# Performance work log

Hardware: AMD Instinct MI355X
Metric: run time of the kernel (lower is better)

## Reference

```python
import jax, jax.numpy as jnp
import numpy as np

N_NODES = 50000
N_EDGES = 800000
D_IN = 128
D_HID = 256
D_OUT = 256


def setup_inputs() -> dict:
    key = jax.random.key(0)
    ks = jax.random.split(key, 16)
    x = jax.random.normal(ks[0], (N_NODES, D_IN), dtype=jnp.float32)
    src = jax.random.randint(ks[1], (N_EDGES,), 0, N_NODES)
    dst = jax.random.randint(ks[2], (N_EDGES,), 0, N_NODES)

    def w(k, fan_in, fan_out):
        return jax.random.normal(k, (fan_in, fan_out), dtype=jnp.float32) / np.sqrt(fan_in)

    return {
        "x": x, "src": src, "dst": dst,
        "Ws0": w(ks[3], D_IN, D_HID), "Wn0": w(ks[4], D_IN, D_HID), "b0": jnp.zeros((D_HID,), jnp.float32),
        "Ws1": w(ks[5], D_HID, D_HID), "Wn1": w(ks[6], D_HID, D_HID), "b1": jnp.zeros((D_HID,), jnp.float32),
        "Ws2": w(ks[7], D_HID, D_OUT), "Wn2": w(ks[8], D_HID, D_OUT), "b2": jnp.zeros((D_OUT,), jnp.float32),
    }


def _sage_layer(h, src, dst, Ws, Wn, b, n_nodes):
    # mean aggregation: gather src features per edge, segment-sum into dst, divide by in-degree
    msg_sum = jax.ops.segment_sum(h[src], dst, num_segments=n_nodes)          # [N, d]
    deg = jax.ops.segment_sum(jnp.ones((src.shape[0],), h.dtype), dst, num_segments=n_nodes)
    h_neigh = msg_sum / jnp.maximum(deg, 1.0)[:, None]                        # zero in-degree -> 0
    return jax.nn.relu(h @ Ws + h_neigh @ Wn + b)


def reference(x, src, dst, Ws0, Wn0, b0, Ws1, Wn1, b1, Ws2, Wn2, b2):
    n = x.shape[0]
    h = _sage_layer(x, src, dst, Ws0, Wn0, b0, n)
    h = _sage_layer(h, src, dst, Ws1, Wn1, b1, n)
    h = _sage_layer(h, src, dst, Ws2, Wn2, b2, n)
    return h
```

## Files before the change

### kernel.cpp

```cpp
#include <hip/hip_runtime.h>
#include <hip/hip_bf16.h>

#define NN 50000
#define NE 800000
#define NB 782
#define BCAP 1536
#define OVFCAP 4096
#define RADIX_BLOCKS 128

typedef __attribute__((ext_vector_type(8))) _Float16 half8v;
typedef __attribute__((ext_vector_type(4))) _Float16 half4v;
typedef __attribute__((ext_vector_type(2))) _Float16 half2v;
typedef __attribute__((ext_vector_type(4))) float f32x4;

__device__ __forceinline__ void gload_lds16(const void* g, void* l) {
  __builtin_amdgcn_global_load_lds((const __attribute__((address_space(1))) void*)g,
                                   (__attribute__((address_space(3))) void*)l, 16, 0, 0);
}
__device__ __forceinline__ void vm_wait5() {
  asm volatile("s_waitcnt vmcnt(5)" ::: "memory");
  __builtin_amdgcn_sched_barrier(0);
}
__device__ __forceinline__ void vm_wait0() {
  asm volatile("s_waitcnt vmcnt(0)" ::: "memory");
  __builtin_amdgcn_sched_barrier(0);
}
__device__ __forceinline__ void barx() {
  __builtin_amdgcn_sched_barrier(0);
  __builtin_amdgcn_s_barrier();
  __builtin_amdgcn_sched_barrier(0);
}

__global__ void k_zero(int* __restrict__ p, int n) {
  int i = blockIdx.x * blockDim.x + threadIdx.x;
  if (i < n) p[i] = 0;
}

__global__ __launch_bounds__(256) void k_radix(const int* __restrict__ src,
                                               const int* __restrict__ dst,
                                               int* __restrict__ bcur,
                                               uint* __restrict__ pairs,
                                               int* __restrict__ cnt,
                                               int* __restrict__ ovfn,
                                               uint* __restrict__ ovf) {
  __shared__ int hist[NB];
  __shared__ int lbase[NB];
  const int tid = threadIdx.x;
  const int chunk = (NE + RADIX_BLOCKS - 1) / RADIX_BLOCKS;
  const int e0 = blockIdx.x * chunk;
  const int e1 = min(e0 + chunk, NE);
  for (int i = tid; i < NB; i += 256) hist[i] = 0;
  __syncthreads();
  for (int e = e0 + tid; e < e1; e += 256) atomicAdd(&hist[dst[e] >> 6], 1);
  __syncthreads();
  for (int i = tid; i < NB; i += 256) {
    int h = hist[i];
    lbase[i] = h ? atomicAdd(&bcur[i], h) : 0;
    hist[i] = 0;
  }
  __syncthreads();
  for (int e = e0 + tid; e < e1; e += 256) {
    int d = dst[e], s = src[e];
    int b = d >> 6;
    int p = lbase[b] + atomicAdd(&hist[b], 1);
    if (p < BCAP) {
      pairs[(size_t)b * BCAP + p] = ((uint)s << 6) | (uint)(d & 63);
    } else {
      int oi = atomicAdd(ovfn, 1);
      if (oi < OVFCAP) ovf[oi] = ((uint)d << 16) | (uint)s;
      atomicAdd(&cnt[d], 1);
    }
  }
}

__global__ __launch_bounds__(256) void k_countb(const int* __restrict__ bcur,
                                                const uint* __restrict__ pairs,
                                                int* __restrict__ cnt) {
  __shared__ int lc[64];
  const int b = blockIdx.x;
  if (threadIdx.x < 64) lc[threadIdx.x] = 0;
  __syncthreads();
  const int m = min(bcur[b], BCAP);
  for (int e = threadIdx.x; e < m; e += 256)
    atomicAdd(&lc[pairs[(size_t)b * BCAP + e] & 63], 1);
  __syncthreads();
  if (threadIdx.x < 64) {
    int node = b * 64 + threadIdx.x;
    int v = lc[threadIdx.x];
    if (node < NN && v) atomicAdd(&cnt[node], v);
  }
}

__global__ __launch_bounds__(1024) void k_scan(int* __restrict__ cnt, int* __restrict__ rowptr) {
  __shared__ int wsum[16];
  __shared__ int woff[16];
  __shared__ int tot;
  const int tid = threadIdx.x;
  const int lane = tid & 63;
  const int w = tid >> 6;
  int running = 0;
  for (int base = 0; base < NN; base += 4096) {
    const int i4 = (base >> 2) + tid;
    int4 v = make_int4(0, 0, 0, 0);
    if (i4 * 4 < NN) v = reinterpret_cast<const int4*>(cnt)[i4];
    const int tsum = v.x + v.y + v.z + v.w;
    int x = tsum;
#pragma unroll
    for (int off = 1; off < 64; off <<= 1) {
      int t = __shfl_up(x, off);
      if (lane >= off) x += t;
    }
    if (lane == 63) wsum[w] = x;
    __syncthreads();
    if (w == 0) {
      int s = (lane < 16) ? wsum[lane] : 0;
#pragma unroll
      for (int off = 1; off < 16; off <<= 1) {
        int t = __shfl_up(s, off);
        if (lane >= off) s += t;
      }
      if (lane < 16) woff[lane] = s - wsum[lane];
      if (lane == 15) tot = s;
    }
    __syncthreads();
    if (i4 * 4 < NN) {
      int excl = running + woff[w] + (x - tsum);
      int4 r;
      r.x = excl;
      r.y = excl + v.x;
      r.z = r.y + v.y;
      r.w = r.z + v.z;
      reinterpret_cast<int4*>(rowptr)[i4] = r;
      reinterpret_cast<int4*>(cnt)[i4] = r;
    }
    running += tot;
    __syncthreads();
  }
  if (tid == 0) rowptr[NN] = running;
}

__global__ __launch_bounds__(256) void k_fillb(const int* __restrict__ bcur,
                                               const uint* __restrict__ pairs,
                                               int* __restrict__ cursor,
                                               int* __restrict__ col) {
  const int b = blockIdx.x;
  const int m = min(bcur[b], BCAP);
  for (int e = threadIdx.x; e < m; e += 256) {
    uint u = pairs[(size_t)b * BCAP + e];
    int node = b * 64 + (int)(u & 63);
    int p = atomicAdd(&cursor[node], 1);
    col[p] = (int)(u >> 6);
  }
}

__global__ void k_fillovf(const int* __restrict__ ovfn, const uint* __restrict__ ovf,
                          int* __restrict__ cursor, int* __restrict__ col) {
  int n = min(*ovfn, OVFCAP);
  for (int i = threadIdx.x; i < n; i += 256) {
    uint u = ovf[i];
    int p = atomicAdd(&cursor[u >> 16], 1);
    col[p] = (int)(u & 0xFFFFu);
  }
}

__global__ void k_wpack(const float* __restrict__ W, _Float16* __restrict__ Wp, int K) {
  int t = blockIdx.x * blockDim.x + threadIdx.x;
  if (t >= K * 32) return;
  int l = t & 63;
  int c = (t >> 6) & 15;
  int kb = t >> 10;
  int row = c * 16 + (l & 15);
  int k = kb * 32 + (l >> 4) * 8;
  half8v o;
#pragma unroll
  for (int i = 0; i < 8; ++i) o[i] = (_Float16)W[(size_t)(k + i) * 256 + row];
  *reinterpret_cast<half8v*>(Wp + (size_t)t * 8) = o;
}

__global__ void k_split16(const float* __restrict__ x, _Float16* __restrict__ X16) {
  int t = blockIdx.x * blockDim.x + threadIdx.x;
  if (t >= NN * 16) return;
  const float* p = x + (size_t)t * 8;
  float4 v0 = *reinterpret_cast<const float4*>(p);
  float4 v1 = *reinterpret_cast<const float4*>(p + 4);
  half8v o;
  o[0] = (_Float16)v0.x; o[1] = (_Float16)v0.y; o[2] = (_Float16)v0.z; o[3] = (_Float16)v0.w;
  o[4] = (_Float16)v1.x; o[5] = (_Float16)v1.y; o[6] = (_Float16)v1.z; o[7] = (_Float16)v1.w;
  *reinterpret_cast<half8v*>(X16 + (size_t)t * 8) = o;
}

__global__ __launch_bounds__(256) void k_agg_x16(const float* __restrict__ x,
                                                 const int* __restrict__ rowptr,
                                                 const int* __restrict__ col,
                                                 _Float16* __restrict__ N) {
  const int lane = threadIdx.x & 63;
  const int n = blockIdx.x * 4 + (threadIdx.x >> 6);
  if (n >= NN) return;
  const int start = rowptr[n];
  const int end = rowptr[n + 1];
  float a0 = 0.f, a1 = 0.f;
  for (int base = start; base < end; base += 64) {
    int e = base + lane;
    int c = (e < end) ? col[e] : 0;
    int m = min(64, end - base);
    int t = 0;
    for (; t + 3 < m; t += 4) {
      int c0 = __shfl(c, t), c1 = __shfl(c, t + 1), c2 = __shfl(c, t + 2), c3 = __shfl(c, t + 3);
      float2 v0 = *reinterpret_cast<const float2*>(x + (size_t)c0 * 128 + lane * 2);
      float2 v1 = *reinterpret_cast<const float2*>(x + (size_t)c1 * 128 + lane * 2);
      float2 v2 = *reinterpret_cast<const float2*>(x + (size_t)c2 * 128 + lane * 2);
      float2 v3 = *reinterpret_cast<const float2*>(x + (size_t)c3 * 128 + lane * 2);
      a0 += v0.x + v1.x + v2.x + v3.x;
      a1 += v0.y + v1.y + v2.y + v3.y;
    }
    for (; t < m; ++t) {
      int cs = __shfl(c, t);
      float2 v = *reinterpret_cast<const float2*>(x + (size_t)cs * 128 + lane * 2);
      a0 += v.x;
      a1 += v.y;
    }
  }
  int deg = end - start;
  float sc = 1.0f / (float)(deg > 0 ? deg : 1);
  half2v o;
  o[0] = (_Float16)(a0 * sc);
  o[1] = (_Float16)(a1 * sc);
  *reinterpret_cast<half2v*>(N + (size_t)n * 128 + lane * 2) = o;
}

__global__ __launch_bounds__(256) void k_agg16(const _Float16* __restrict__ H,
                                               const int* __restrict__ rowptr,
                                               const int* __restrict__ col,
                                               _Float16* __restrict__ N) {
  const int lane = threadIdx.x & 63;
  const int n = blockIdx.x * 4 + (threadIdx.x >> 6);
  if (n >= NN) return;
  const int start = rowptr[n];
  const int end = rowptr[n + 1];
  float a0 = 0.f, a1 = 0.f, a2 = 0.f, a3 = 0.f;
  for (int base = start; base < end; base += 64) {
    int e = base + lane;
    int c = (e < end) ? col[e] : 0;
    int m = min(64, end - base);
    int t = 0;
    for (; t + 3 < m; t += 4) {
      int c0 = __shfl(c, t), c1 = __shfl(c, t + 1), c2 = __shfl(c, t + 2), c3 = __shfl(c, t + 3);
      half4v v0 = *reinterpret_cast<const half4v*>(H + (size_t)c0 * 256 + lane * 4);
      half4v v1 = *reinterpret_cast<const half4v*>(H + (size_t)c1 * 256 + lane * 4);
      half4v v2 = *reinterpret_cast<const half4v*>(H + (size_t)c2 * 256 + lane * 4);
      half4v v3 = *reinterpret_cast<const half4v*>(H + (size_t)c3 * 256 + lane * 4);
      a0 += (float)v0[0] + (float)v1[0] + (float)v2[0] + (float)v3[0];
      a1 += (float)v0[1] + (float)v1[1] + (float)v2[1] + (float)v3[1];
      a2 += (float)v0[2] + (float)v1[2] + (float)v2[2] + (float)v3[2];
      a3 += (float)v0[3] + (float)v1[3] + (float)v2[3] + (float)v3[3];
    }
    for (; t < m; ++t) {
      int cs = __shfl(c, t);
      half4v v = *reinterpret_cast<const half4v*>(H + (size_t)cs * 256 + lane * 4);
      a0 += (float)v[0];
      a1 += (float)v[1];
      a2 += (float)v[2];
      a3 += (float)v[3];
    }
  }
  int deg = end - start;
  float sc = 1.0f / (float)(deg > 0 ? deg : 1);
  half4v o;
  o[0] = (_Float16)(a0 * sc);
  o[1] = (_Float16)(a1 * sc);
  o[2] = (_Float16)(a2 * sc);
  o[3] = (_Float16)(a3 * sc);
  *reinterpret_cast<half4v*>(N + (size_t)n * 256 + lane * 4) = o;
}

__global__ __launch_bounds__(256) void k_mfma16(
    const _Float16* __restrict__ A1, const _Float16* __restrict__ A2,
    const _Float16* __restrict__ W1p, const _Float16* __restrict__ W2p,
    const float* __restrict__ bias, int K,
    _Float16* __restrict__ outH, float* __restrict__ outF) {
  __shared__ _Float16 LDS[20480];
  const int tid = threadIdx.x;
  const int w = tid >> 6;
  const int lane = tid & 63;
  const int lrow = lane & 15;
  const int kg8 = (lane >> 4) * 8;
  const int m0 = blockIdx.x * 64;
  const int nk = K >> 5;
  const int nsteps = nk * 2;

  f32x4 acc[4][4];
#pragma unroll
  for (int i = 0; i < 4; ++i)
#pragma unroll
    for (int j = 0; j < 4; ++j) acc[i][j] = (f32x4){0.f, 0.f, 0.f, 0.f};

  int arowi = m0 + w * 16 + lrow;
  const size_t arow = (size_t)(arowi < NN ? arowi : NN - 1);

#define STAGE(S, B)                                                            \
  {                                                                            \
    const _Float16* Ap = ((S) >= nk) ? A2 : A1;                                \
    const _Float16* Wp = ((S) >= nk) ? W2p : W1p;                              \
    const int sl = ((S) >= nk) ? (S) - nk : (S);                               \
    gload_lds16(Ap + arow * K + (sl << 5) + kg8,                               \
                (void*)&LDS[(B) * 10240 + w * 512]);                           \
    const _Float16* wsrc = Wp + (size_t)(sl * 16 + w * 4) * 512 + lane * 8;    \
    _Pragma("unroll") for (int j = 0; j < 4; ++j)                              \
        gload_lds16(wsrc + j * 512,                                            \
                    (void*)&LDS[(B) * 10240 + 2048 + (w * 4 + j) * 512]);      \
  }

#define COMPUTE(B)                                                             \
  {                                                                            \
    half8v af[4];                                                              \
    _Pragma("unroll") for (int rf = 0; rf < 4; ++rf)                           \
        af[rf] = *reinterpret_cast<const half8v*>(                             \
            &LDS[(B) * 10240 + rf * 512 + lane * 8]);                          \
    _Pragma("unroll") for (int cf = 0; cf < 4; ++cf) {                         \
      half8v bf = *reinterpret_cast<const half8v*>(                            \
          &LDS[(B) * 10240 + 2048 + (w * 4 + cf) * 512 + lane * 8]);           \
      _Pragma("unroll") for (int rf = 0; rf < 4; ++rf)                         \
          acc[rf][cf] = __builtin_amdgcn_mfma_f32_16x16x32_f16(                \
              af[rf], bf, acc[rf][cf], 0, 0, 0);                               \
    }                                                                          \
  }

  STAGE(0, 0);
  STAGE(1, 1);
  vm_wait5();
  barx();
  for (int s = 0; s < nsteps; ++s) {
    COMPUTE(s & 1);
    barx();
    if (s + 2 < nsteps) {
      STAGE(s + 2, s & 1);
      vm_wait5();
    } else {
      vm_wait0();
    }
    barx();
  }
#undef STAGE
#undef COMPUTE

  const int rquad = (lane >> 4) * 4;
  if (outF) {
#pragma unroll
    for (int cf = 0; cf < 4; ++cf) {
      const int colc = w * 64 + cf * 16 + lrow;
      const float bb = bias[colc];
#pragma unroll
      for (int rf = 0; rf < 4; ++rf)
#pragma unroll
        for (int j = 0; j < 4; ++j) {
          const int row = m0 + rf * 16 + rquad + j;
          if (row < NN) {
            float v = acc[rf][cf][j] + bb;
            outF[(size_t)row * 256 + colc] = v > 0.f ? v : 0.f;
          }
        }
    }
  } else {
#pragma unroll
    for (int cf = 0; cf < 4; ++cf) {
      const int colc = w * 64 + cf * 16 + lrow;
      const float bb = bias[colc];
#pragma unroll
      for (int rf = 0; rf < 4; ++rf)
#pragma unroll
        for (int j = 0; j < 4; ++j) {
          float v = acc[rf][cf][j] + bb;
          LDS[(rf * 16 + rquad + j) * 264 + colc] = (_Float16)(v > 0.f ? v : 0.f);
        }
    }
    __syncthreads();
    const int row = tid >> 2;
    const int q = tid & 3;
    if (m0 + row < NN) {
#pragma unroll
      for (int it = 0; it < 8; ++it)
        *reinterpret_cast<half8v*>(outH + (size_t)(m0 + row) * 256 + q * 64 + it * 8) =
            *reinterpret_cast<const half8v*>(&LDS[row * 264 + q * 64 + it * 8]);
    }
  }
}

extern "C" void kernel_launch(void* const* d_in, const int* in_sizes, int n_in,
                              void* d_out, int out_size, void* d_ws, size_t ws_size,
                              hipStream_t stream) {
  const float* x   = (const float*)d_in[0];
  const int* src   = (const int*)d_in[1];
  const int* dst   = (const int*)d_in[2];
  const float* Ws0 = (const float*)d_in[3];
  const float* Wn0 = (const float*)d_in[4];
  const float* b0  = (const float*)d_in[5];
  const float* Ws1 = (const float*)d_in[6];
  const float* Wn1 = (const float*)d_in[7];
  const float* b1  = (const float*)d_in[8];
  const float* Ws2 = (const float*)d_in[9];
  const float* Wn2 = (const float*)d_in[10];
  const float* b2  = (const float*)d_in[11];
  float* out = (float*)d_out;

  char* ws = (char*)d_ws;
  size_t off = 0;
  auto alloc = [&](size_t bytes) {
    void* p = ws + off;
    off = (off + bytes + 255) & ~(size_t)255;
    return p;
  };
  _Float16* X16 = (_Float16*)alloc((size_t)NN * 128 * 2);
  _Float16* H   = (_Float16*)alloc((size_t)NN * 256 * 2);
  _Float16* Nb  = (_Float16*)alloc((size_t)NN * 256 * 2);
  int* rowptr = (int*)alloc((size_t)(NN + 1) * sizeof(int));
  const int ZN = 50048 + 1024 + 64;
  int* meta = (int*)alloc((size_t)ZN * sizeof(int));
  int* cnt  = meta;
  int* bcur = meta + 50048;
  int* ovfn = meta + 50048 + 1024;
  int* col    = (int*)alloc((size_t)NE * sizeof(int));
  uint* pairs = (uint*)alloc((size_t)NB * BCAP * sizeof(uint));
  uint* ovf   = (uint*)alloc((size_t)OVFCAP * sizeof(uint));
  _Float16* W0s = (_Float16*)alloc(256 * 128 * 2);
  _Float16* W0n = (_Float16*)alloc(256 * 128 * 2);
  _Float16* W1s = (_Float16*)alloc(256 * 256 * 2);
  _Float16* W1n = (_Float16*)alloc(256 * 256 * 2);
  _Float16* W2s = (_Float16*)alloc(256 * 256 * 2);
  _Float16* W2n = (_Float16*)alloc(256 * 256 * 2);

  k_zero<<<(ZN + 1023) / 1024, 1024, 0, stream>>>(meta, ZN);
  k_radix<<<RADIX_BLOCKS, 256, 0, stream>>>(src, dst, bcur, pairs, cnt, ovfn, ovf);
  k_countb<<<NB, 256, 0, stream>>>(bcur, pairs, cnt);
  k_scan<<<1, 1024, 0, stream>>>(cnt, rowptr);
  k_fillb<<<NB, 256, 0, stream>>>(bcur, pairs, cnt, col);
  k_fillovf<<<1, 256, 0, stream>>>(ovfn, ovf, cnt, col);

  k_wpack<<<16, 256, 0, stream>>>(Ws0, W0s, 128);
  k_wpack<<<16, 256, 0, stream>>>(Wn0, W0n, 128);
  k_wpack<<<32, 256, 0, stream>>>(Ws1, W1s, 256);
  k_wpack<<<32, 256, 0, stream>>>(Wn1, W1n, 256);
  k_wpack<<<32, 256, 0, stream>>>(Ws2, W2s, 256);
  k_wpack<<<32, 256, 0, stream>>>(Wn2, W2n, 256);

  k_split16<<<(NN * 16 + 255) / 256, 256, 0, stream>>>(x, X16);

  const int aggGrid = (NN + 3) / 4;
  const int gemmGrid = (NN + 63) / 64;

  k_agg_x16<<<aggGrid, 256, 0, stream>>>(x, rowptr, col, Nb);
  k_mfma16<<<gemmGrid, 256, 0, stream>>>(X16, Nb, W0s, W0n, b0, 128, H, nullptr);
  k_agg16<<<aggGrid, 256, 0, stream>>>(H, rowptr, col, Nb);
  k_mfma16<<<gemmGrid, 256, 0, stream>>>(H, Nb, W1s, W1n, b1, 256, H, nullptr);
  k_agg16<<<aggGrid, 256, 0, stream>>>(H, rowptr, col, Nb);
  k_mfma16<<<gemmGrid, 256, 0, stream>>>(H, Nb, W2s, W2n, b2, 256, nullptr, out);
}
```

Measured before the change: 433.7 us.

## Slice features into 32-column planes for cache-friendly aggregation and 16-bit col indices

Result: slower. 589.0 us (+35.8%).

```diff
diff --git a/kernel.cpp b/kernel.cpp
--- a/kernel.cpp
+++ b/kernel.cpp
@@ -7,10 +7,10 @@
 #define BCAP 1536
 #define OVFCAP 4096
 #define RADIX_BLOCKS 128
+#define NBX 12500
 
 typedef __attribute__((ext_vector_type(8))) _Float16 half8v;
 typedef __attribute__((ext_vector_type(4))) _Float16 half4v;
-typedef __attribute__((ext_vector_type(2))) _Float16 half2v;
 typedef __attribute__((ext_vector_type(4))) float f32x4;
 
 __device__ __forceinline__ void gload_lds16(const void* g, void* l) {
@@ -142,24 +142,24 @@
 __global__ __launch_bounds__(256) void k_fillb(const int* __restrict__ bcur,
                                                const uint* __restrict__ pairs,
                                                int* __restrict__ cursor,
-                                               int* __restrict__ col) {
+                                               ushort* __restrict__ col) {
   const int b = blockIdx.x;
   const int m = min(bcur[b], BCAP);
   for (int e = threadIdx.x; e < m; e += 256) {
     uint u = pairs[(size_t)b * BCAP + e];
     int node = b * 64 + (int)(u & 63);
     int p = atomicAdd(&cursor[node], 1);
-    col[p] = (int)(u >> 6);
+    col[p] = (ushort)(u >> 6);
   }
 }
 
 __global__ void k_fillovf(const int* __restrict__ ovfn, const uint* __restrict__ ovf,
-                          int* __restrict__ cursor, int* __restrict__ col) {
+                          int* __restrict__ cursor, ushort* __restrict__ col) {
   int n = min(*ovfn, OVFCAP);
   for (int i = threadIdx.x; i < n; i += 256) {
     uint u = ovf[i];
     int p = atomicAdd(&cursor[u >> 16], 1);
-    col[p] = (int)(u & 0xFFFFu);
+    col[p] = (ushort)(u & 0xFFFFu);
   }
 }
 
@@ -177,100 +177,60 @@
   *reinterpret_cast<half8v*>(Wp + (size_t)t * 8) = o;
 }
 
-__global__ void k_split16(const float* __restrict__ x, _Float16* __restrict__ X16) {
+__global__ void k_split16(const float* __restrict__ x, _Float16* __restrict__ Xs) {
   int t = blockIdx.x * blockDim.x + threadIdx.x;
   if (t >= NN * 16) return;
-  const float* p = x + (size_t)t * 8;
+  int r = t >> 4;
+  int qq = t & 15;
+  const float* p = x + (size_t)r * 128 + qq * 8;
   float4 v0 = *reinterpret_cast<const float4*>(p);
   float4 v1 = *reinterpret_cast<const float4*>(p + 4);
   half8v o;
   o[0] = (_Float16)v0.x; o[1] = (_Float16)v0.y; o[2] = (_Float16)v0.z; o[3] = (_Float16)v0.w;
   o[4] = (_Float16)v1.x; o[5] = (_Float16)v1.y; o[6] = (_Float16)v1.z; o[7] = (_Float16)v1.w;
-  *reinterpret_cast<half8v*>(X16 + (size_t)t * 8) = o;
-}
-
-__global__ __launch_bounds__(256) void k_agg_x16(const float* __restrict__ x,
-                                                 const int* __restrict__ rowptr,
-                                                 const int* __restrict__ col,
-                                                 _Float16* __restrict__ N) {
+  int s = qq >> 2;
+  *reinterpret_cast<half8v*>(Xs + ((size_t)s * NN + r) * 32 + (qq & 3) * 8) = o;
+}
+
+__global__ __launch_bounds__(256) void k_aggs(const _Float16* __restrict__ Hs,
+                                              const int* __restrict__ rowptr,
+                                              const ushort* __restrict__ col,
+                                              _Float16* __restrict__ Ns) {
+  const int s = blockIdx.x / NBX;
+  const int nb = blockIdx.x - s * NBX;
+  const int n = nb * 4 + (threadIdx.x >> 6);
   const int lane = threadIdx.x & 63;
-  const int n = blockIdx.x * 4 + (threadIdx.x >> 6);
-  if (n >= NN) return;
-  const int start = rowptr[n];
-  const int end = rowptr[n + 1];
-  float a0 = 0.f, a1 = 0.f;
-  for (int base = start; base < end; base += 64) {
-    int e = base + lane;
-    int c = (e < end) ? col[e] : 0;
-    int m = min(64, end - base);
-    int t = 0;
-    for (; t + 3 < m; t += 4) {
-      int c0 = __shfl(c, t), c1 = __shfl(c, t + 1), c2 = __shfl(c, t + 2), c3 = __shfl(c, t + 3);
-      float2 v0 = *reinterpret_cast<const float2*>(x + (size_t)c0 * 128 + lane * 2);
-      float2 v1 = *reinterpret_cast<const float2*>(x + (size_t)c1 * 128 + lane * 2);
-      float2 v2 = *reinterpret_cast<const float2*>(x + (size_t)c2 * 128 + lane * 2);
-      float2 v3 = *reinterpret_cast<const float2*>(x + (size_t)c3 * 128 + lane * 2);
-      a0 += v0.x + v1.x + v2.x + v3.x;
-      a1 += v0.y + v1.y + v2.y + v3.y;
-    }
-    for (; t < m; ++t) {
-      int cs = __shfl(c, t);
-      float2 v = *reinterpret_cast<const float2*>(x + (size_t)cs * 128 + lane * 2);
-      a0 += v.x;
-      a1 += v.y;
-    }
-  }
-  int deg = end - start;
-  float sc = 1.0f / (float)(deg > 0 ? deg : 1);
-  half2v o;
-  o[0] = (_Float16)(a0 * sc);
-  o[1] = (_Float16)(a1 * sc);
-  *reinterpret_cast<half2v*>(N + (size_t)n * 128 + lane * 2) = o;
-}
-
-__global__ __launch_bounds__(256) void k_agg16(const _Float16* __restrict__ H,
-                                               const int* __restrict__ rowptr,
-                                               const int* __restrict__ col,
-                                               _Float16* __restrict__ N) {
-  const int lane = threadIdx.x & 63;
-  const int n = blockIdx.x * 4 + (threadIdx.x >> 6);
-  if (n >= NN) return;
+  const int g = lane >> 3;
+  const int o = lane & 7;
+  const _Float16* base = Hs + (size_t)s * NN * 32;
   const int start = rowptr[n];
   const int end = rowptr[n + 1];
   float a0 = 0.f, a1 = 0.f, a2 = 0.f, a3 = 0.f;
-  for (int base = start; base < end; base += 64) {
-    int e = base + lane;
-    int c = (e < end) ? col[e] : 0;
-    int m = min(64, end - base);
-    int t = 0;
-    for (; t + 3 < m; t += 4) {
-      int c0 = __shfl(c, t), c1 = __shfl(c, t + 1), c2 = __shfl(c, t + 2), c3 = __shfl(c, t + 3);
-      half4v v0 = *reinterpret_cast<const half4v*>(H + (size_t)c0 * 256 + lane * 4);
-      half4v v1 = *reinterpret_cast<const half4v*>(H + (size_t)c1 * 256 + lane * 4);
-      half4v v2 = *reinterpret_cast<const half4v*>(H + (size_t)c2 * 256 + lane * 4);
-      half4v v3 = *reinterpret_cast<const half4v*>(H + (size_t)c3 * 256 + lane * 4);
-      a0 += (float)v0[0] + (float)v1[0] + (float)v2[0] + (float)v3[0];
-      a1 += (float)v0[1] + (float)v1[1] + (float)v2[1] + (float)v3[1];
-      a2 += (float)v0[2] + (float)v1[2] + (float)v2[2] + (float)v3[2];
-      a3 += (float)v0[3] + (float)v1[3] + (float)v2[3] + (float)v3[3];
-    }
-    for (; t < m; ++t) {
-      int cs = __shfl(c, t);
-      half4v v = *reinterpret_cast<const half4v*>(H + (size_t)cs * 256 + lane * 4);
-      a0 += (float)v[0];
-      a1 += (float)v[1];
-      a2 += (float)v[2];
-      a3 += (float)v[3];
-    }
-  }
-  int deg = end - start;
-  float sc = 1.0f / (float)(deg > 0 ? deg : 1);
-  half4v o;
-  o[0] = (_Float16)(a0 * sc);
-  o[1] = (_Float16)(a1 * sc);
-  o[2] = (_Float16)(a2 * sc);
-  o[3] = (_Float16)(a3 * sc);
-  *reinterpret_cast<half4v*>(N + (size_t)n * 256 + lane * 4) = o;
+  for (int e = start + g; e < end; e += 8) {
+    int c = col[e];
+    half4v v = *reinterpret_cast<const half4v*>(base + (size_t)c * 32 + o * 4);
+    a0 += (float)v[0];
+    a1 += (float)v[1];
+    a2 += (float)v[2];
+    a3 += (float)v[3];
+  }
+#pragma unroll
+  for (int m = 8; m < 64; m <<= 1) {
+    a0 += __shfl_xor(a0, m);
+    a1 += __shfl_xor(a1, m);
+    a2 += __shfl_xor(a2, m);
+    a3 += __shfl_xor(a3, m);
+  }
+  if (lane < 8) {
+    int deg = end - start;
+    float sc = 1.0f / (float)(deg > 0 ? deg : 1);
+    half4v ov;
+    ov[0] = (_Float16)(a0 * sc);
+    ov[1] = (_Float16)(a1 * sc);
+    ov[2] = (_Float16)(a2 * sc);
+    ov[3] = (_Float16)(a3 * sc);
+    *reinterpret_cast<half4v*>(Ns + ((size_t)s * NN + n) * 32 + lane * 4) = ov;
+  }
 }
 
 __global__ __launch_bounds__(256) void k_mfma16(
@@ -302,7 +262,7 @@
     const _Float16* Ap = ((S) >= nk) ? A2 : A1;                                \
     const _Float16* Wp = ((S) >= nk) ? W2p : W1p;                              \
     const int sl = ((S) >= nk) ? (S) - nk : (S);                               \
-    gload_lds16(Ap + arow * K + (sl << 5) + kg8,                               \
+    gload_lds16(Ap + ((size_t)sl * NN + arow) * 32 + kg8,                      \
                 (void*)&LDS[(B) * 10240 + w * 512]);                           \
     const _Float16* wsrc = Wp + (size_t)(sl * 16 + w * 4) * 512 + lane * 8;    \
     _Pragma("unroll") for (int j = 0; j < 4; ++j)                              \
@@ -374,13 +334,15 @@
         }
     }
     __syncthreads();
-    const int row = tid >> 2;
-    const int q = tid & 3;
-    if (m0 + row < NN) {
-#pragma unroll
-      for (int it = 0; it < 8; ++it)
-        *reinterpret_cast<half8v*>(outH + (size_t)(m0 + row) * 256 + q * 64 + it * 8) =
-            *reinterpret_cast<const half8v*>(&LDS[row * 264 + q * 64 + it * 8]);
+    if (m0 + lane < NN) {
+#pragma unroll
+      for (int ss = 0; ss < 2; ++ss) {
+        const int s = w * 2 + ss;
+#pragma unroll
+        for (int it = 0; it < 4; ++it)
+          *reinterpret_cast<half8v*>(outH + ((size_t)s * NN + m0 + lane) * 32 + it * 8) =
+              *reinterpret_cast<const half8v*>(&LDS[lane * 264 + s * 32 + it * 8]);
+      }
     }
   }
 }
@@ -409,16 +371,16 @@
     off = (off + bytes + 255) & ~(size_t)255;
     return p;
   };
-  _Float16* X16 = (_Float16*)alloc((size_t)NN * 128 * 2);
-  _Float16* H   = (_Float16*)alloc((size_t)NN * 256 * 2);
-  _Float16* Nb  = (_Float16*)alloc((size_t)NN * 256 * 2);
+  _Float16* Xs = (_Float16*)alloc((size_t)NN * 128 * 2);
+  _Float16* Hs = (_Float16*)alloc((size_t)NN * 256 * 2);
+  _Float16* Ns = (_Float16*)alloc((size_t)NN * 256 * 2);
   int* rowptr = (int*)alloc((size_t)(NN + 1) * sizeof(int));
   const int ZN = 50048 + 1024 + 64;
   int* meta = (int*)alloc((size_t)ZN * sizeof(int));
   int* cnt  = meta;
   int* bcur = meta + 50048;
   int* ovfn = meta + 50048 + 1024;
-  int* col    = (int*)alloc((size_t)NE * sizeof(int));
+  ushort* col = (ushort*)alloc((size_t)NE * sizeof(ushort));
   uint* pairs = (uint*)alloc((size_t)NB * BCAP * sizeof(uint));
   uint* ovf   = (uint*)alloc((size_t)OVFCAP * sizeof(uint));
   _Float16* W0s = (_Float16*)alloc(256 * 128 * 2);
@@ -442,15 +404,14 @@
   k_wpack<<<32, 256, 0, stream>>>(Ws2, W2s, 256);
   k_wpack<<<32, 256, 0, stream>>>(Wn2, W2n, 256);
 
-  k_split16<<<(NN * 16 + 255) / 256, 256, 0, stream>>>(x, X16);
-
-  const int aggGrid = (NN + 3) / 4;
+  k_split16<<<(NN * 16 + 255) / 256, 256, 0, stream>>>(x, Xs);
+
   const int gemmGrid = (NN + 63) / 64;
 
-  k_agg_x16<<<aggGrid, 256, 0, stream>>>(x, rowptr, col, Nb);
-  k_mfma16<<<gemmGrid, 256, 0, stream>>>(X16, Nb, W0s, W0n, b0, 128, H, nullptr);
-  k_agg16<<<aggGrid, 256, 0, stream>>>(H, rowptr, col, Nb);
-  k_mfma16<<<gemmGrid, 256, 0, stream>>>(H, Nb, W1s, W1n, b1, 256, H, nullptr);
-  k_agg16<<<aggGrid, 256, 0, stream>>>(H, rowptr, col, Nb);
-  k_mfma16<<<gemmGrid, 256, 0, stream>>>(H, Nb, W2s, W2n, b2, 256, nullptr, out);
-}
+  k_aggs<<<NBX * 4, 256, 0, stream>>>(Xs, rowptr, col, Ns);
+  k_mfma16<<<gemmGrid, 256, 0, stream>>>(Xs, Ns, W0s, W0n, b0, 128, Hs, nullptr);
+  k_aggs<<<NBX * 8, 256, 0, stream>>>(Hs, rowptr, col, Ns);
+  k_mfma16<<<gemmGrid, 256, 0, stream>>>(Hs, Ns, W1s, W1n, b1, 256, Hs, nullptr);
+  k_aggs<<<NBX * 8, 256, 0, stream>>>(Hs, rowptr, col, Ns);
+  k_mfma16<<<gemmGrid, 256, 0, stream>>>(Hs, Ns, W2s, W2n, b2, 256, nullptr, out);
+}
```
